# Optimization experiments

Measured on AMD Instinct MI355X. Metric: run time of the kernel, lower is better.

The kernel has to match this reference:

```python
import jax, jax.numpy as jnp
import numpy as np

# yolov5 non_max_suppression defaults (from forward's input_parameters.get defaults)
CONF_THRES = 0.25
IOU_THRES = 0.45
MAX_DET = 1000        # max detections returned per image
TOP_K = 4096          # fixed candidate count entering greedy NMS (jit-friendly stand-in for max_nms)
MAX_WH = 7680.0       # per-class box offset so NMS is class-aware (yolov5 trick)


def setup_inputs() -> dict:
    key = jax.random.key(0)
    k1, k2, k3, k4 = jax.random.split(key, 4)
    B, N, NC = 16, 25200, 80  # 640x640 yolov5 -> 25200 anchors, 80 COCO classes
    xy = jax.random.uniform(k1, (B, N, 2)) * 640.0            # box centers in pixels
    wh = jax.random.uniform(k2, (B, N, 2)) * 160.0 + 4.0       # box sizes
    obj = jax.random.uniform(k3, (B, N, 1))                    # objectness
    cls = jax.random.uniform(k4, (B, N, NC))                   # class scores
    pred = jnp.concatenate([xy, wh, obj, cls], axis=-1)        # [B, N, 85]
    return {"pred": pred}


def _xywh2xyxy(x):
    xy, wh = x[..., :2], x[..., 2:4]
    return jnp.concatenate([xy - wh * 0.5, xy + wh * 0.5], axis=-1)


def _iou_one_vs_all(box, boxes):
    # box [4], boxes [K,4], xyxy
    lt = jnp.maximum(box[:2], boxes[:, :2])
    rb = jnp.minimum(box[2:], boxes[:, 2:])
    wh = jnp.clip(rb - lt, 0.0)
    inter = wh[:, 0] * wh[:, 1]
    a1 = (box[2] - box[0]) * (box[3] - box[1])
    a2 = (boxes[:, 2] - boxes[:, 0]) * (boxes[:, 3] - boxes[:, 1])
    return inter / (a1 + a2 - inter + 1e-7)


def _nms_single(pred):
    # pred [N, 5+nc] raw yolov5 output for one image
    obj = pred[:, 4:5]
    scores_all = pred[:, 5:] * obj                 # conf = obj_conf * cls_conf
    conf = scores_all.max(axis=-1)                 # best-class confidence [N]
    cls = scores_all.argmax(axis=-1).astype(pred.dtype)
    boxes = _xywh2xyxy(pred[:, :4])                # [N,4] xyxy

    valid = conf > CONF_THRES
    s = jnp.where(valid, conf, -1.0)
    order = jnp.argsort(-s)[:TOP_K]                # top candidates by score
    b = boxes[order]                               # [K,4]
    sc = s[order]                                  # [K]
    c = cls[order]                                 # [K]
    ob = b + c[:, None] * MAX_WH                   # class-offset boxes for class-aware NMS

    ar = jnp.arange(TOP_K)

    def step(supp, i):
        alive = (~supp[i]) & (sc[i] > 0.0)
        iou = _iou_one_vs_all(ob[i], ob)
        supp = supp | (alive & (iou > IOU_THRES) & (ar > i))
        return supp, alive

    _, keep = jax.lax.scan(step, jnp.zeros(TOP_K, dtype=bool), ar)

    fs = jnp.where(keep, sc, -1.0)
    idx = jnp.argsort(-fs)[:MAX_DET]               # kept boxes, score-sorted
    det = jnp.concatenate([b[idx], fs[idx][:, None], c[idx][:, None]], axis=-1)  # [max_det,6]
    ok = fs[idx] > 0.0
    return jnp.where(ok[:, None], det, 0.0)        # zero-padded [max_det, 6] (x1,y1,x2,y2,conf,cls)


def reference(pred):
    # [B, max_det, 6] padded detections per image
    return jax.vmap(_nms_single)(pred)
```

## Files before the change

kernel.cpp:

```cpp
#include <hip/hip_runtime.h>

#define BATCH  16
#define NPRED  25200
#define NCLS   80
#define CDIM   85
#define TOPK   4096
#define NPAD   28672
#define NCHUNK 7
#define MAXDET 1000
#define CONF_T 0.25f
#define IOU_T  0.45f
#define MAXWH  7680.0f

typedef unsigned long long u64;
typedef unsigned int u32;
typedef unsigned short u16;
typedef unsigned char u8;


__device__ __forceinline__ void cx_u64(u64* a, int i, int p, bool desc) {
    u64 x = a[i], y = a[p];
    if (desc ? (x < y) : (x > y)) { a[i] = y; a[p] = x; }
}

__device__ __forceinline__ void sort4096_desc_u64(u64* a) {
    const int tid = threadIdx.x;
    for (int k = 2; k <= 4096; k <<= 1) {
        for (int j = k >> 1; j > 0; j >>= 1) {
            __syncthreads();
#pragma unroll
            for (int t = 0; t < 2; ++t) {
                int q = (t << 10) | tid;
                int i = ((q & ~(j - 1)) << 1) | (q & (j - 1));
                cx_u64(a, i, i | j, (i & k) == 0);
            }
        }
    }
    __syncthreads();
}

__device__ __forceinline__ void merge4096_desc_u64(u64* a) {
    const int tid = threadIdx.x;
    for (int j = 2048; j > 0; j >>= 1) {
        __syncthreads();
#pragma unroll
        for (int t = 0; t < 2; ++t) {
            int q = (t << 10) | tid;
            int i = ((q & ~(j - 1)) << 1) | (q & (j - 1));
            cx_u64(a, i, i | j, true);
        }
    }
    __syncthreads();
}


__global__ __launch_bounds__(256) void k1_score(const float* __restrict__ pred,
                                                u64* __restrict__ keys) {
    const int lane = threadIdx.x & 63;
    const int l16 = lane & 15;
    const long long gw = (long long)blockIdx.x * 4 + (threadIdx.x >> 6);
    const long long rowIdx = gw * 4 + (lane >> 4);
    const int b = (int)(rowIdx / NPAD);
    const int n = (int)(rowIdx - (long long)b * NPAD);
    u64 key = 0ull;
    if (n < NPRED) {
        const float* row = pred + ((long long)b * NPRED + n) * CDIM;
        float obj = row[4];
        u64 m = 0ull;
#pragma unroll
        for (int k = 0; k < 5; ++k) {
            int c = l16 + 16 * k;
            float v = row[5 + c] * obj;
            u64 mk = ((u64)(__float_as_uint(v) | 0x80000000u) << 32) | (u64)(u32)(NCLS - 1 - c);
            if (mk > m) m = mk;
        }
#pragma unroll
        for (int o = 8; o > 0; o >>= 1) {
            u64 other = __shfl_xor(m, o, 64);
            if (other > m) m = other;
        }
        float best = __uint_as_float((u32)(m >> 32) & 0x7FFFFFFFu);
        int cls = (NCLS - 1) - (int)(m & 0x7Fu);
        float s = (best > CONF_T) ? best : -1.0f;
        u32 u = __float_as_uint(s);
        u32 ord = (u & 0x80000000u) ? ~u : (u | 0x80000000u);
        key = ((u64)ord << 32) | ((u64)(u32)(NPAD - 1 - n) << 7) | (u64)(u32)cls;
    }
    if (l16 == 0) keys[(long long)b * NPAD + n] = key;
}


__global__ __launch_bounds__(1024) void k2a_sortchunk(u64* __restrict__ keys) {
    __shared__ u64 arr[4096];
    const int tid = threadIdx.x;
    u64* kb = keys + (long long)blockIdx.x * 4096;
#pragma unroll
    for (int t = 0; t < 4; ++t) { int i = (t << 10) | tid; arr[i] = kb[i]; }
    sort4096_desc_u64(arr);
#pragma unroll
    for (int t = 0; t < 4; ++t) { int i = (t << 10) | tid; kb[i] = arr[i]; }
}


__global__ __launch_bounds__(1024) void k2m_merge(u64* __restrict__ keys, int stride) {
    __shared__ u64 arr[4096];
    const int tid = threadIdx.x;
    const int b = blockIdx.x;
    const int c0 = blockIdx.y * 2 * stride;
    const u64* A = keys + (long long)b * NPAD + (long long)c0 * 4096;
    const u64* B = keys + (long long)b * NPAD + (long long)(c0 + stride) * 4096;
#pragma unroll
    for (int t = 0; t < 4; ++t) {
        int i = (t << 10) | tid;
        u64 x = A[i], y = B[4095 - i];
        arr[i] = (x > y) ? x : y;
    }
    merge4096_desc_u64(arr);
    u64* O = keys + (long long)b * NPAD + (long long)c0 * 4096;
#pragma unroll
    for (int t = 0; t < 4; ++t) { int i = (t << 10) | tid; O[i] = arr[i]; }
}


__global__ __launch_bounds__(256) void k3a_build(const float* __restrict__ pred,
                                                 const u64* __restrict__ keys,
                                                 float4* __restrict__ ob,
                                                 u8* __restrict__ clsb,
                                                 u32* __restrict__ count) {
    const int idx = blockIdx.x * 256 + threadIdx.x;
    const int b = idx >> 12;
    const int r = idx & 4095;
    u64 key = keys[(long long)b * NPAD + r];
    u32 hi = (u32)(key >> 32);
    u8 c = 0xFF;
    if (hi > 0x80000000u) {
        int n = (NPAD - 1) - (int)((key >> 7) & 0x7FFFu);
        int ci = (int)(key & 0x7Fu);
        const float* row = pred + ((long long)b * NPRED + n) * CDIM;
        float x = row[0], y = row[1], w = row[2], h = row[3];
        float off = (float)ci * MAXWH;
        float4 o;
        o.x = (x - w * 0.5f) + off;
        o.y = (y - h * 0.5f) + off;
        o.z = (x + w * 0.5f) + off;
        o.w = (y + h * 0.5f) + off;
        ob[idx] = o;
        c = (u8)ci;
        atomicAdd(&count[b * NCLS + ci], 1u);
    }
    clsb[idx] = c;
}


__global__ __launch_bounds__(64) void k3g_gather(const u8* __restrict__ clsb,
                                                 const u32* __restrict__ count,
                                                 u32* __restrict__ startg,
                                                 u16* __restrict__ segIdx) {
    const int b = blockIdx.x;
    const int c = blockIdx.y;
    const int lane = threadIdx.x;
    u32 s = (lane < c) ? count[b * NCLS + lane] : 0u;
    if (lane + 64 < c) s += count[b * NCLS + 64 + lane];
#pragma unroll
    for (int o = 32; o > 0; o >>= 1) s += __shfl_xor(s, o, 64);
    if (lane == 0) startg[b * NCLS + c] = s;
    const u32 base = (u32)b * 4096u;
    u32 pos = s;
    const u64 lt = (1ull << lane) - 1ull;
    for (int it = 0; it < 64; ++it) {
        u8 cc = clsb[base + it * 64 + lane];
        u64 m = __ballot(cc == (u8)c);
        if (cc == (u8)c) {
            int ofs = __popcll(m & lt);
            segIdx[base + pos + ofs] = (u16)(it * 64 + lane);
        }
        pos += (u32)__popcll(m);
    }
}


__global__ __launch_bounds__(64) void k3n_nms(const float4* __restrict__ ob,
                                              const u16* __restrict__ segIdx,
                                              const u32* __restrict__ count,
                                              const u32* __restrict__ startg,
                                              u8* __restrict__ keep,
                                              u8* gsupp_) {
    const int b = blockIdx.x;
    const int c = blockIdx.y;
    const int lane = threadIdx.x;
    const int n = (int)count[b * NCLS + c];
    if (n == 0) return;
    const u32 base = startg[b * NCLS + c];
    __shared__ float4 sbox[1024];
    __shared__ u16 sidx[1024];
    __shared__ u8 ssupp_[1024];
    volatile u8* ssupp = ssupp_;
    volatile u8* gsupp = gsupp_ + b * 4096 + base;
    const float4* obb = ob + b * 4096;
    const u16* seg = segIdx + b * 4096 + base;

    for (int j = lane; j < n && j < 1024; j += 64) {
        int r = seg[j];
        sidx[j] = (u16)r;
        sbox[j] = obb[r];
        ssupp_[j] = 0;
    }
    __syncthreads();

    {
#pragma clang fp contract(off)
        for (int ii = 0; ii < n; ++ii) {
            bool sup = (ii < 1024) ? (ssupp[ii] != 0) : (gsupp[ii] != 0);
            if (sup) continue;
            int ri = (ii < 1024) ? (int)sidx[ii] : (int)seg[ii];
            if (lane == 0) keep[b * 4096 + ri] = 1;
            float4 bi = (ii < 1024) ? sbox[ii] : obb[seg[ii]];
            float a1 = (bi.z - bi.x) * (bi.w - bi.y);
            for (int jj = ii + 1 + lane; jj < n; jj += 64) {
                float4 bj = (jj < 1024) ? sbox[jj] : obb[seg[jj]];
                float ltx = fmaxf(bi.x, bj.x);
                float lty = fmaxf(bi.y, bj.y);
                float rbx = fminf(bi.z, bj.z);
                float rby = fminf(bi.w, bj.w);
                float ww = fmaxf(rbx - ltx, 0.0f);
                float hh = fmaxf(rby - lty, 0.0f);
                float inter = ww * hh;
                float a2 = (bj.z - bj.x) * (bj.w - bj.y);
                float iou = inter / (((a1 + a2) - inter) + 1e-7f);
                if (iou > IOU_T) {
                    if (jj < 1024) ssupp[jj] = 1; else gsupp[jj] = 1;
                }
            }
            __syncthreads();
        }
    }
}


__global__ __launch_bounds__(256) void k3o_out(const float* __restrict__ pred,
                                               const u64* __restrict__ keys,
                                               const u8* __restrict__ keep,
                                               float* __restrict__ out) {
    const int b = blockIdx.x;
    const int tid = threadIdx.x;
    __shared__ u64 words[64];
    __shared__ int wpre[64];
    float* outb = out + (long long)b * MAXDET * 6;
    for (int i = tid; i < MAXDET * 6; i += 256) outb[i] = 0.0f;
    const u8* kp = keep + b * 4096;
    if (tid < 64) {
        u64 w = 0ull;
        const u64* k8 = (const u64*)(kp + tid * 64);
#pragma unroll
        for (int q = 0; q < 8; ++q) {
            u64 v = k8[q];
#pragma unroll
            for (int bb = 0; bb < 8; ++bb)
                if ((v >> (8 * bb)) & 0xFFull) w |= 1ull << (q * 8 + bb);
        }
        words[tid] = w;
    }
    __syncthreads();
    if (tid == 0) {
        int run = 0;
        for (int t = 0; t < 64; ++t) { wpre[t] = run; run += __popcll(words[t]); }
    }
    __syncthreads();
    const u64* kb = keys + (long long)b * NPAD;
    for (int r = tid; r < 4096; r += 256) {
        int wd = r >> 6;
        if ((words[wd] >> (r & 63)) & 1ull) {
            int pos = wpre[wd] + __popcll(words[wd] & ((1ull << (r & 63)) - 1ull));
            if (pos < MAXDET) {
                u64 key = kb[r];
                u32 hi = (u32)(key >> 32);
                int n = (NPAD - 1) - (int)((key >> 7) & 0x7FFFu);
                const float* row = pred + ((long long)b * NPRED + n) * CDIM;
                float x = row[0], y = row[1], w2 = row[2], h = row[3];
                float* o = outb + pos * 6;
                o[0] = x - w2 * 0.5f;
                o[1] = y - h * 0.5f;
                o[2] = x + w2 * 0.5f;
                o[3] = y + h * 0.5f;
                o[4] = __uint_as_float(hi & 0x7FFFFFFFu);
                o[5] = (float)(key & 0x7Fu);
            }
        }
    }
}


extern "C" void kernel_launch(void* const* d_in, const int* in_sizes, int n_in,
                              void* d_out, int out_size, void* d_ws, size_t ws_size,
                              hipStream_t stream) {
    const float* pred = (const float*)d_in[0];
    float* out = (float*)d_out;

    char* ws = (char*)d_ws;
    u64* keys   = (u64*)ws;
    float4* ob  = (float4*)(ws + 3670016);
    u8* clsb    = (u8*)(ws + 4718592);
    u16* segIdx = (u16*)(ws + 4784128);
    u32* startg = (u32*)(ws + 4915200);
    u32* count  = (u32*)(ws + 4920320);
    u8* keep    = (u8*)(ws + 4925440);
    u8* gsupp   = (u8*)(ws + 4990976);
    (void)hipMemsetAsync(ws + 4920320, 0, 136192, stream);

    hipLaunchKernelGGL(k1_score, dim3(BATCH * NPAD / 16), dim3(256), 0, stream, pred, keys);
    hipLaunchKernelGGL(k2a_sortchunk, dim3(BATCH * NCHUNK), dim3(1024), 0, stream, keys);
    hipLaunchKernelGGL(k2m_merge, dim3(BATCH, 3), dim3(1024), 0, stream, keys, 1);
    hipLaunchKernelGGL(k2m_merge, dim3(BATCH, 2), dim3(1024), 0, stream, keys, 2);
    hipLaunchKernelGGL(k2m_merge, dim3(BATCH, 1), dim3(1024), 0, stream, keys, 4);
    hipLaunchKernelGGL(k3a_build, dim3(BATCH * TOPK / 256), dim3(256), 0, stream,
                       pred, keys, ob, clsb, count);
    hipLaunchKernelGGL(k3g_gather, dim3(BATCH, NCLS), dim3(64), 0, stream,
                       clsb, count, startg, segIdx);
    hipLaunchKernelGGL(k3n_nms, dim3(BATCH, NCLS), dim3(64), 0, stream,
                       ob, segIdx, count, startg, keep, gsupp);
    hipLaunchKernelGGL(k3o_out, dim3(BATCH), dim3(256), 0, stream, pred, keys, keep, out);
}
```

Before: 315.6 us.

## Use register and wave-shuffle bitonic stages for small strides in chunk sort and merge

The bitonic sort and merge of 4096-key chunks now keep four keys per thread in registers. Compare-exchange stages with strides below 256 run through in-register swaps and cross-lane shuffles within a 64-wide wavefront, and only the larger strides go through shared memory with block barriers. This cuts the number of __syncthreads and LDS round-trips per sort. The cost is more 64-bit shuffle traffic and extra register pressure at 1024 threads per block.

After: 304.6 us. 3.5% less time.

```diff
diff --git a/kernel.cpp b/kernel.cpp
--- a/kernel.cpp
+++ b/kernel.cpp
@@ -17,40 +17,108 @@
 typedef unsigned short u16;
 typedef unsigned char u8;
 
+__device__ __forceinline__ u64 umax64(u64 a, u64 b) { return a > b ? a : b; }
+__device__ __forceinline__ u64 umin64(u64 a, u64 b) { return a < b ? a : b; }
 
 __device__ __forceinline__ void cx_u64(u64* a, int i, int p, bool desc) {
     u64 x = a[i], y = a[p];
     if (desc ? (x < y) : (x > y)) { a[i] = y; a[p] = x; }
 }
 
-__device__ __forceinline__ void sort4096_desc_u64(u64* a) {
+
+__device__ void hybrid_sort4096_desc(u64 r[4], u64* a) {
     const int tid = threadIdx.x;
     for (int k = 2; k <= 4096; k <<= 1) {
-        for (int j = k >> 1; j > 0; j >>= 1) {
+        if (k >= 512) {
+            int jmax = (k >> 1) > 2048 ? 2048 : (k >> 1);
+#pragma unroll
+            for (int e = 0; e < 4; ++e) a[4 * tid + e] = r[e];
             __syncthreads();
-#pragma unroll
-            for (int t = 0; t < 2; ++t) {
-                int q = (t << 10) | tid;
-                int i = ((q & ~(j - 1)) << 1) | (q & (j - 1));
-                cx_u64(a, i, i | j, (i & k) == 0);
+            for (int j = jmax; j >= 256; j >>= 1) {
+#pragma unroll
+                for (int t2 = 0; t2 < 2; ++t2) {
+                    int q = (t2 << 10) | tid;
+                    int i = ((q & ~(j - 1)) << 1) | (q & (j - 1));
+                    cx_u64(a, i, i | j, (i & k) == 0);
+                }
+                __syncthreads();
             }
-        }
-    }
+#pragma unroll
+            for (int e = 0; e < 4; ++e) r[e] = a[4 * tid + e];
+            __syncthreads();
+        }
+        {
+            int jstart = (k >> 1) > 128 ? 128 : (k >> 1);
+            bool desc = (((4 * tid) & k) == 0);
+            for (int j = jstart; j >= 4; j >>= 1) {
+                int m = j >> 2;
+                bool take_max = (((tid & m) == 0) == desc);
+#pragma unroll
+                for (int e = 0; e < 4; ++e) {
+                    u64 v = __shfl_xor(r[e], m, 64);
+                    r[e] = take_max ? umax64(r[e], v) : umin64(r[e], v);
+                }
+            }
+        }
+        if (k >= 4) {
+            bool desc = (((4 * tid) & k) == 0);
+            u64 x0 = r[0], x2 = r[2];
+            r[0] = desc ? umax64(x0, x2) : umin64(x0, x2);
+            r[2] = desc ? umin64(x0, x2) : umax64(x0, x2);
+            u64 x1 = r[1], x3 = r[3];
+            r[1] = desc ? umax64(x1, x3) : umin64(x1, x3);
+            r[3] = desc ? umin64(x1, x3) : umax64(x1, x3);
+        }
+        {
+            bool d01 = (((4 * tid + 0) & k) == 0);
+            bool d23 = (((4 * tid + 2) & k) == 0);
+            u64 x0 = r[0], x1 = r[1];
+            r[0] = d01 ? umax64(x0, x1) : umin64(x0, x1);
+            r[1] = d01 ? umin64(x0, x1) : umax64(x0, x1);
+            u64 x2 = r[2], x3 = r[3];
+            r[2] = d23 ? umax64(x2, x3) : umin64(x2, x3);
+            r[3] = d23 ? umin64(x2, x3) : umax64(x2, x3);
+        }
+    }
+}
+
+__device__ void hybrid_merge4096_desc(u64 r[4], u64* a) {
+    const int tid = threadIdx.x;
+#pragma unroll
+    for (int e = 0; e < 4; ++e) a[4 * tid + e] = r[e];
     __syncthreads();
-}
-
-__device__ __forceinline__ void merge4096_desc_u64(u64* a) {
-    const int tid = threadIdx.x;
-    for (int j = 2048; j > 0; j >>= 1) {
-        __syncthreads();
-#pragma unroll
-        for (int t = 0; t < 2; ++t) {
-            int q = (t << 10) | tid;
+    for (int j = 2048; j >= 256; j >>= 1) {
+#pragma unroll
+        for (int t2 = 0; t2 < 2; ++t2) {
+            int q = (t2 << 10) | tid;
             int i = ((q & ~(j - 1)) << 1) | (q & (j - 1));
             cx_u64(a, i, i | j, true);
         }
-    }
-    __syncthreads();
+        __syncthreads();
+    }
+#pragma unroll
+    for (int e = 0; e < 4; ++e) r[e] = a[4 * tid + e];
+    for (int j = 128; j >= 4; j >>= 1) {
+        int m = j >> 2;
+        bool take_max = ((tid & m) == 0);
+#pragma unroll
+        for (int e = 0; e < 4; ++e) {
+            u64 v = __shfl_xor(r[e], m, 64);
+            r[e] = take_max ? umax64(r[e], v) : umin64(r[e], v);
+        }
+    }
+    {
+        u64 x0 = r[0], x2 = r[2];
+        r[0] = umax64(x0, x2); r[2] = umin64(x0, x2);
+        u64 x1 = r[1], x3 = r[3];
+        r[1] = umax64(x1, x3); r[3] = umin64(x1, x3);
+    }
+    {
+        u64 x0 = r[0], x1 = r[1];
+        r[0] = umax64(x0, x1); r[1] = umin64(x0, x1);
+        u64 x2 = r[2], x3 = r[3];
+        r[2] = umax64(x2, x3); r[3] = umin64(x2, x3);
+    }
 }
 
 
@@ -91,34 +159,35 @@
 
 
 __global__ __launch_bounds__(1024) void k2a_sortchunk(u64* __restrict__ keys) {
-    __shared__ u64 arr[4096];
+    __shared__ u64 a[4096];
     const int tid = threadIdx.x;
     u64* kb = keys + (long long)blockIdx.x * 4096;
-#pragma unroll
-    for (int t = 0; t < 4; ++t) { int i = (t << 10) | tid; arr[i] = kb[i]; }
-    sort4096_desc_u64(arr);
-#pragma unroll
-    for (int t = 0; t < 4; ++t) { int i = (t << 10) | tid; kb[i] = arr[i]; }
+    u64 r[4];
+#pragma unroll
+    for (int e = 0; e < 4; ++e) r[e] = kb[4 * tid + e];
+    hybrid_sort4096_desc(r, a);
+#pragma unroll
+    for (int e = 0; e < 4; ++e) kb[4 * tid + e] = r[e];
 }
 
 
 __global__ __launch_bounds__(1024) void k2m_merge(u64* __restrict__ keys, int stride) {
-    __shared__ u64 arr[4096];
+    __shared__ u64 a[4096];
     const int tid = threadIdx.x;
     const int b = blockIdx.x;
     const int c0 = blockIdx.y * 2 * stride;
     const u64* A = keys + (long long)b * NPAD + (long long)c0 * 4096;
     const u64* B = keys + (long long)b * NPAD + (long long)(c0 + stride) * 4096;
-#pragma unroll
-    for (int t = 0; t < 4; ++t) {
-        int i = (t << 10) | tid;
-        u64 x = A[i], y = B[4095 - i];
-        arr[i] = (x > y) ? x : y;
-    }
-    merge4096_desc_u64(arr);
+    u64 r[4];
+#pragma unroll
+    for (int e = 0; e < 4; ++e) {
+        int i = 4 * tid + e;
+        r[e] = umax64(A[i], B[4095 - i]);
+    }
+    hybrid_merge4096_desc(r, a);
     u64* O = keys + (long long)b * NPAD + (long long)c0 * 4096;
 #pragma unroll
-    for (int t = 0; t < 4; ++t) { int i = (t << 10) | tid; O[i] = arr[i]; }
+    for (int e = 0; e < 4; ++e) O[4 * tid + e] = r[e];
 }
 
 
```
